# Performance work log

Measured on AMD Instinct MI355X. Metric: run time of the kernel, lower is better.

The kernel has to match this reference:

```python
import jax, jax.numpy as jnp
import numpy as np

B, D, H = 2048, 64, 512  # batch, state dim, vf hidden dim
IS_DIFFUSION = True      # vf output divided by 2.0 as in CNF.forward


def setup_inputs() -> dict:
    key = jax.random.key(0)
    ks = jax.random.split(key, 8)

    def lin(k, fi, fo):
        return jax.random.normal(k, (fi, fo), jnp.float32) / np.float32(np.sqrt(fi))

    return {
        "t": jax.random.uniform(ks[0], (1,), jnp.float32),      # scalar time, kept as [1]
        "x": jax.random.normal(ks[1], (B, D + 1), jnp.float32),  # last col = logp channel
        "W1": lin(ks[2], D + 1, H),
        "b1": jax.random.normal(ks[3], (H,), jnp.float32) * 0.01,
        "W2": lin(ks[4], H, H),
        "b2": jax.random.normal(ks[5], (H,), jnp.float32) * 0.01,
        "W3": lin(ks[6], H, D),
        "b3": jax.random.normal(ks[7], (D,), jnp.float32) * 0.01,
    }


def reference(t, x, W1, b1, W2, b2, W3, b3):
    scale = 2.0 if IS_DIFFUSION else 1.0
    xd = x[..., :-1]  # [B, D] -- drop augmented log-density channel

    def vf_single(xi):  # R^D -> R^D vector field, t and params closed over
        h = jnp.concatenate([xi, t])           # [D+1] (time-conditioned input)
        h = jnp.tanh(h @ W1 + b1)
        h = jnp.tanh(h @ W2 + b2)
        return (h @ W3 + b3) / scale

    dx = jax.vmap(vf_single)(xd)  # [B, D]
    # exact divergence: trace of per-sample Jacobian via reverse-mode (matches torch jacrev)
    div = jax.vmap(lambda xi: jnp.trace(jax.jacrev(vf_single)(xi)))(xd)  # [B]
    return jnp.concatenate([dx, div[:, None]], axis=-1)  # [B, D+1]
```

## Files before the change

### kernel.cpp

```cpp
#include <hip/hip_runtime.h>


constexpr int HD = 512;
constexpr int DD = 64;
constexpr int SB = 8;
constexpr int NB = 2048 / SB;

typedef __attribute__((ext_vector_type(8))) short bf16x8;
typedef __attribute__((ext_vector_type(4))) float f32x4;

__device__ inline unsigned short f2bf(float f) {
    union { float f; unsigned u; } v; v.f = f;
    return (unsigned short)((v.u + 0x7fffu + ((v.u >> 16) & 1u)) >> 16);
}
__device__ inline float fast_tanh(float xx) {
    float e = __expf(2.f * xx);
    return 1.f - 2.f / (e + 1.f);
}

__global__ __launch_bounds__(64) void cnf_pack_kernel(
    const float* __restrict__ W1, const float* __restrict__ W2,
    const float* __restrict__ W3, unsigned short* __restrict__ Bpack)
{
    __shared__ float w1s[64][33];
    __shared__ float w3s[16][65];
    const int b = blockIdx.x;
    const int mat = b >> 9, t = (b >> 4) & 31, kk = b & 15;
    const int l = threadIdx.x;
    const int q = l >> 4, nl = l & 15;
    const int n = t * 16 + nl;
    unsigned short o[8];
    if (mat == 0) {
#pragma unroll
        for (int j = 0; j < 8; ++j) {
            int k = kk * 32 + q * 8 + j;
            o[j] = f2bf(W2[k * HD + n]);
        }
    } else {
        for (int e = l; e < 64 * 32; e += 64) {
            int i = e >> 5, kl = e & 31;
            w1s[i][kl] = W1[i * HD + kk * 32 + kl];
        }
        for (int e = l; e < 16 * 64; e += 64) {
            int nn = e >> 6, i = e & 63;
            w3s[nn][i] = W3[(t * 16 + nn) * DD + i];
        }
        __syncthreads();
#pragma unroll
        for (int j = 0; j < 8; ++j) {
            int kl = q * 8 + j;
            float m = 0.f;
#pragma unroll 8
            for (int i = 0; i < 64; ++i) m += w1s[i][kl] * w3s[nl][i];
            o[j] = f2bf(W2[(kk * 32 + kl) * HD + n] * m);
        }
    }
    uint4 pk;
    pk.x = (unsigned)o[0] | ((unsigned)o[1] << 16);
    pk.y = (unsigned)o[2] | ((unsigned)o[3] << 16);
    pk.z = (unsigned)o[4] | ((unsigned)o[5] << 16);
    pk.w = (unsigned)o[6] | ((unsigned)o[7] << 16);
    reinterpret_cast<uint4*>(Bpack)[b * 64 + l] = pk;
}

__global__ __launch_bounds__(512, 2) void cnf_fused_kernel(
    const float* __restrict__ tptr, const float* __restrict__ x,
    const float* __restrict__ W1, const float* __restrict__ b1,
    const float* __restrict__ b2v, const float* __restrict__ W3,
    const float* __restrict__ b3, const unsigned short* __restrict__ Bpack,
    float* __restrict__ out)
{
    __shared__ float4 xsv[65 * 2];
    __shared__ unsigned short A_lds[16][520];
    __shared__ float4 h2v[HD * 2];
    __shared__ float4 divred[8][2];
    __shared__ float sm_b2[HD];

    const int tid  = threadIdx.x;
    const int s0   = blockIdx.x * SB;
    const int wave = tid >> 6, lane = tid & 63;

    {
        const float tval = tptr[0];
        for (int e = tid; e < SB * 65; e += 512) {
            int s = e / 65, i = e % 65;
            reinterpret_cast<float*>(xsv)[i * SB + s] =
                (i == DD) ? tval : x[(s0 + s) * 65 + i];
        }
        sm_b2[tid] = b2v[tid];
    }
    __syncthreads();

    {
        const int u = tid;
        const float bb = b1[u];
        float2 a0 = {bb, bb}, a1 = {bb, bb}, a2 = {bb, bb}, a3 = {bb, bb};
        for (int ib = 0; ib < 64; ib += 8) {
            float w[8];
#pragma unroll
            for (int qq = 0; qq < 8; ++qq) w[qq] = W1[(ib + qq) * HD + u];
#pragma unroll
            for (int qq = 0; qq < 8; ++qq) {
                float4 p = xsv[2 * (ib + qq)], r = xsv[2 * (ib + qq) + 1];
                a0.x += p.x * w[qq]; a0.y += p.y * w[qq];
                a1.x += p.z * w[qq]; a1.y += p.w * w[qq];
                a2.x += r.x * w[qq]; a2.y += r.y * w[qq];
                a3.x += r.z * w[qq]; a3.y += r.w * w[qq];
            }
        }
        {
            float w = W1[64 * HD + u];
            float4 p = xsv[128], r = xsv[129];
            a0.x += p.x * w; a0.y += p.y * w;
            a1.x += p.z * w; a1.y += p.w * w;
            a2.x += r.x * w; a2.y += r.y * w;
            a3.x += r.z * w; a3.y += r.w * w;
        }
        float h[8] = {fast_tanh(a0.x), fast_tanh(a0.y), fast_tanh(a1.x), fast_tanh(a1.y),
                      fast_tanh(a2.x), fast_tanh(a2.y), fast_tanh(a3.x), fast_tanh(a3.y)};
#pragma unroll
        for (int s = 0; s < 8; ++s) {
            A_lds[s][u]     = f2bf(h[s]);
            A_lds[8 + s][u] = f2bf(1.f - h[s] * h[s]);
        }
    }
    __syncthreads();

    f32x4 cw[4], cg[4];
#pragma unroll
    for (int i = 0; i < 4; ++i) { cw[i] = (f32x4){0,0,0,0}; cg[i] = (f32x4){0,0,0,0}; }
    {
        const unsigned short* arow = &A_lds[lane & 15][0];
        const int aoff = (lane >> 4) * 8;
        const bf16x8* bw = reinterpret_cast<const bf16x8*>(Bpack)
                         + (size_t)(wave * 64) * 64 + lane;
        const bf16x8* bg = bw + 32768;

        bf16x8 pA[16], pB[16];
        auto loadSB = [&](bf16x8* d, int kk) {
#pragma unroll
            for (int i = 0; i < 4; ++i) {
                d[i]      = bw[kk * 64 + i * 1024];
                d[4 + i]  = bg[kk * 64 + i * 1024];
                d[8 + i]  = bw[(kk + 1) * 64 + i * 1024];
                d[12 + i] = bg[(kk + 1) * 64 + i * 1024];
            }
        };
        auto mfmaSB = [&](const bf16x8* d, int kk) {
            bf16x8 af0 = *reinterpret_cast<const bf16x8*>(arow + kk * 32 + aoff);
#pragma unroll
            for (int i = 0; i < 4; ++i)
                cw[i] = __builtin_amdgcn_mfma_f32_16x16x32_bf16(af0, d[i], cw[i], 0, 0, 0);
#pragma unroll
            for (int i = 0; i < 4; ++i)
                cg[i] = __builtin_amdgcn_mfma_f32_16x16x32_bf16(af0, d[4 + i], cg[i], 0, 0, 0);
            bf16x8 af1 = *reinterpret_cast<const bf16x8*>(arow + (kk + 1) * 32 + aoff);
#pragma unroll
            for (int i = 0; i < 4; ++i)
                cw[i] = __builtin_amdgcn_mfma_f32_16x16x32_bf16(af1, d[8 + i], cw[i], 0, 0, 0);
#pragma unroll
            for (int i = 0; i < 4; ++i)
                cg[i] = __builtin_amdgcn_mfma_f32_16x16x32_bf16(af1, d[12 + i], cg[i], 0, 0, 0);
        };

        loadSB(pA, 0);
#pragma unroll
        for (int kb = 0; kb < 8; ++kb) {
            bf16x8* cur = (kb & 1) ? pB : pA;
            bf16x8* nxt = (kb & 1) ? pA : pB;
            if (kb < 7) loadSB(nxt, (kb + 1) * 2);
            mfmaSB(cur, kb * 2);
        }
    }

    {
        const int q = lane >> 4;
        const int src = (lane >= 32) ? lane - 32 : lane;
        float4 dp = {0.f, 0.f, 0.f, 0.f};
#pragma unroll
        for (int i = 0; i < 4; ++i) {
            const int m = wave * 64 + i * 16 + (lane & 15);
            const float bb = sm_b2[m];
            float4 hv;
            hv.x = fast_tanh(cw[i][0] + bb);
            hv.y = fast_tanh(cw[i][1] + bb);
            hv.z = fast_tanh(cw[i][2] + bb);
            hv.w = fast_tanh(cw[i][3] + bb);
            if (lane < 32) h2v[2 * m + q] = hv;
            float h0 = __shfl(hv.x, src), h1s = __shfl(hv.y, src);
            float h2s = __shfl(hv.z, src), h3s = __shfl(hv.w, src);
            dp.x += cg[i][0] * (1.f - h0 * h0);
            dp.y += cg[i][1] * (1.f - h1s * h1s);
            dp.z += cg[i][2] * (1.f - h2s * h2s);
            dp.w += cg[i][3] * (1.f - h3s * h3s);
        }
        if (lane >= 32) {
#pragma unroll
            for (int off = 8; off > 0; off >>= 1) {
                dp.x += __shfl_down(dp.x, off, 16);
                dp.y += __shfl_down(dp.y, off, 16);
                dp.z += __shfl_down(dp.z, off, 16);
                dp.w += __shfl_down(dp.w, off, 16);
            }
            if ((lane & 15) == 0) divred[wave][q - 2] = dp;
        }
    }
    __syncthreads();

    float* opart = reinterpret_cast<float*>(A_lds);

    {
        const int k = lane, part = wave;
        float o[8];
#pragma unroll
        for (int q = 0; q < 8; ++q) o[q] = 0.f;
        const int mb = part * 64;
        for (int mm = 0; mm < 64; mm += 4) {
            float w[4];
#pragma unroll
            for (int q = 0; q < 4; ++q) w[q] = W3[(mb + mm + q) * DD + k];
#pragma unroll
            for (int q = 0; q < 4; ++q) {
                const int m = mb + mm + q;
                float4 ha = h2v[2 * m], hb = h2v[2 * m + 1];
                o[0] += ha.x * w[q]; o[1] += ha.y * w[q];
                o[2] += ha.z * w[q]; o[3] += ha.w * w[q];
                o[4] += hb.x * w[q]; o[5] += hb.y * w[q];
                o[6] += hb.z * w[q]; o[7] += hb.w * w[q];
            }
        }
#pragma unroll
        for (int q = 0; q < 8; ++q) opart[part * 512 + q * 64 + k] = o[q];
    }
    __syncthreads();

    {
        const int s = tid >> 6, k = tid & 63;
        float sum = b3[k];
#pragma unroll
        for (int p = 0; p < 8; ++p) sum += opart[p * 512 + s * 64 + k];
        out[(s0 + s) * 65 + k] = 0.5f * sum;
    }
    if (tid < 8) {
        const int qq = tid >> 2, r = tid & 3;
        float ds = 0.f;
#pragma unroll
        for (int w = 0; w < 8; ++w)
            ds += reinterpret_cast<const float*>(&divred[w][qq])[r];
        out[(s0 + tid) * 65 + DD] = 0.5f * ds;
    }
}

extern "C" void kernel_launch(void* const* d_in, const int* in_sizes, int n_in,
                              void* d_out, int out_size, void* d_ws, size_t ws_size,
                              hipStream_t stream) {
    const float* t  = (const float*)d_in[0];
    const float* x  = (const float*)d_in[1];
    const float* W1 = (const float*)d_in[2];
    const float* b1 = (const float*)d_in[3];
    const float* W2 = (const float*)d_in[4];
    const float* b2 = (const float*)d_in[5];
    const float* W3 = (const float*)d_in[6];
    const float* b3 = (const float*)d_in[7];
    float* out = (float*)d_out;
    unsigned short* Bpack = (unsigned short*)d_ws;

    cnf_pack_kernel<<<1024, 64, 0, stream>>>(W1, W2, W3, Bpack);
    cnf_fused_kernel<<<NB, 512, 0, stream>>>(t, x, W1, b1, b2, W3, b3, Bpack, out);
}
```

Before: 97.81 us.

## Split hidden-layer output dimension across two blocks with atomic accumulation

Each sample group is now handled by two blocks, each computing half of the 512 second-layer hidden units plus their share of the divergence and output projection. Partial results are combined with atomicAdd into an output that is zeroed with a memset first. Launch bounds rise to four blocks per CU to pair with the smaller per-block register and LDS footprint. The aim is more blocks and better occupancy, at the cost of running the first layer twice per sample group, atomic traffic, and an extra memset launch.

```diff
diff --git a/kernel.cpp b/kernel.cpp
--- a/kernel.cpp
+++ b/kernel.cpp
@@ -4,7 +4,7 @@
 constexpr int HD = 512;
 constexpr int DD = 64;
 constexpr int SB = 8;
-constexpr int NB = 2048 / SB;
+constexpr int NBLK = 2 * 2048 / SB;
 
 typedef __attribute__((ext_vector_type(8))) short bf16x8;
 typedef __attribute__((ext_vector_type(4))) float f32x4;
@@ -63,7 +63,7 @@
     reinterpret_cast<uint4*>(Bpack)[b * 64 + l] = pk;
 }
 
-__global__ __launch_bounds__(512, 2) void cnf_fused_kernel(
+__global__ __launch_bounds__(512, 4) void cnf_fused_kernel(
     const float* __restrict__ tptr, const float* __restrict__ x,
     const float* __restrict__ W1, const float* __restrict__ b1,
     const float* __restrict__ b2v, const float* __restrict__ W3,
@@ -72,12 +72,14 @@
 {
     __shared__ float4 xsv[65 * 2];
     __shared__ unsigned short A_lds[16][520];
-    __shared__ float4 h2v[HD * 2];
+    __shared__ float4 h2v[256 * 2];
     __shared__ float4 divred[8][2];
-    __shared__ float sm_b2[HD];
+    __shared__ float sm_b2[256];
 
     const int tid  = threadIdx.x;
-    const int s0   = blockIdx.x * SB;
+    const int sg   = blockIdx.x >> 1;
+    const int q    = blockIdx.x & 1;
+    const int s0   = sg * SB;
     const int wave = tid >> 6, lane = tid & 63;
 
     {
@@ -87,7 +89,7 @@
             reinterpret_cast<float*>(xsv)[i * SB + s] =
                 (i == DD) ? tval : x[(s0 + s) * 65 + i];
         }
-        sm_b2[tid] = b2v[tid];
+        if (tid < 256) sm_b2[tid] = b2v[q * 256 + tid];
     }
     __syncthreads();
 
@@ -126,41 +128,39 @@
     }
     __syncthreads();
 
-    f32x4 cw[4], cg[4];
-#pragma unroll
-    for (int i = 0; i < 4; ++i) { cw[i] = (f32x4){0,0,0,0}; cg[i] = (f32x4){0,0,0,0}; }
+    f32x4 cw[2], cg[2];
+#pragma unroll
+    for (int i = 0; i < 2; ++i) { cw[i] = (f32x4){0,0,0,0}; cg[i] = (f32x4){0,0,0,0}; }
     {
         const unsigned short* arow = &A_lds[lane & 15][0];
         const int aoff = (lane >> 4) * 8;
+        const int t0 = q * 16 + wave * 2;
         const bf16x8* bw = reinterpret_cast<const bf16x8*>(Bpack)
-                         + (size_t)(wave * 64) * 64 + lane;
+                         + (size_t)(t0 * 16) * 64 + lane;
         const bf16x8* bg = bw + 32768;
 
-        bf16x8 pA[16], pB[16];
+        bf16x8 pA[8], pB[8];
         auto loadSB = [&](bf16x8* d, int kk) {
 #pragma unroll
-            for (int i = 0; i < 4; ++i) {
-                d[i]      = bw[kk * 64 + i * 1024];
-                d[4 + i]  = bg[kk * 64 + i * 1024];
-                d[8 + i]  = bw[(kk + 1) * 64 + i * 1024];
-                d[12 + i] = bg[(kk + 1) * 64 + i * 1024];
+            for (int v = 0; v < 2; ++v) {
+#pragma unroll
+                for (int i = 0; i < 2; ++i) {
+                    d[v * 4 + i]     = bw[(kk + v) * 64 + i * 1024];
+                    d[v * 4 + 2 + i] = bg[(kk + v) * 64 + i * 1024];
+                }
             }
         };
         auto mfmaSB = [&](const bf16x8* d, int kk) {
-            bf16x8 af0 = *reinterpret_cast<const bf16x8*>(arow + kk * 32 + aoff);
-#pragma unroll
-            for (int i = 0; i < 4; ++i)
-                cw[i] = __builtin_amdgcn_mfma_f32_16x16x32_bf16(af0, d[i], cw[i], 0, 0, 0);
-#pragma unroll
-            for (int i = 0; i < 4; ++i)
-                cg[i] = __builtin_amdgcn_mfma_f32_16x16x32_bf16(af0, d[4 + i], cg[i], 0, 0, 0);
-            bf16x8 af1 = *reinterpret_cast<const bf16x8*>(arow + (kk + 1) * 32 + aoff);
-#pragma unroll
-            for (int i = 0; i < 4; ++i)
-                cw[i] = __builtin_amdgcn_mfma_f32_16x16x32_bf16(af1, d[8 + i], cw[i], 0, 0, 0);
-#pragma unroll
-            for (int i = 0; i < 4; ++i)
-                cg[i] = __builtin_amdgcn_mfma_f32_16x16x32_bf16(af1, d[12 + i], cg[i], 0, 0, 0);
+#pragma unroll
+            for (int v = 0; v < 2; ++v) {
+                bf16x8 af = *reinterpret_cast<const bf16x8*>(arow + (kk + v) * 32 + aoff);
+#pragma unroll
+                for (int i = 0; i < 2; ++i)
+                    cw[i] = __builtin_amdgcn_mfma_f32_16x16x32_bf16(af, d[v * 4 + i], cw[i], 0, 0, 0);
+#pragma unroll
+                for (int i = 0; i < 2; ++i)
+                    cg[i] = __builtin_amdgcn_mfma_f32_16x16x32_bf16(af, d[v * 4 + 2 + i], cg[i], 0, 0, 0);
+            }
         };
 
         loadSB(pA, 0);
@@ -174,19 +174,19 @@
     }
 
     {
-        const int q = lane >> 4;
+        const int qd = lane >> 4;
         const int src = (lane >= 32) ? lane - 32 : lane;
         float4 dp = {0.f, 0.f, 0.f, 0.f};
 #pragma unroll
-        for (int i = 0; i < 4; ++i) {
-            const int m = wave * 64 + i * 16 + (lane & 15);
-            const float bb = sm_b2[m];
+        for (int i = 0; i < 2; ++i) {
+            const int ml = wave * 32 + i * 16 + (lane & 15);
+            const float bb = sm_b2[ml];
             float4 hv;
             hv.x = fast_tanh(cw[i][0] + bb);
             hv.y = fast_tanh(cw[i][1] + bb);
             hv.z = fast_tanh(cw[i][2] + bb);
             hv.w = fast_tanh(cw[i][3] + bb);
-            if (lane < 32) h2v[2 * m + q] = hv;
+            if (lane < 32) h2v[2 * ml + qd] = hv;
             float h0 = __shfl(hv.x, src), h1s = __shfl(hv.y, src);
             float h2s = __shfl(hv.z, src), h3s = __shfl(hv.w, src);
             dp.x += cg[i][0] * (1.f - h0 * h0);
@@ -202,7 +202,7 @@
                 dp.z += __shfl_down(dp.z, off, 16);
                 dp.w += __shfl_down(dp.w, off, 16);
             }
-            if ((lane & 15) == 0) divred[wave][q - 2] = dp;
+            if ((lane & 15) == 0) divred[wave][qd - 2] = dp;
         }
     }
     __syncthreads();
@@ -213,33 +213,34 @@
         const int k = lane, part = wave;
         float o[8];
 #pragma unroll
-        for (int q = 0; q < 8; ++q) o[q] = 0.f;
-        const int mb = part * 64;
-        for (int mm = 0; mm < 64; mm += 4) {
+        for (int qq = 0; qq < 8; ++qq) o[qq] = 0.f;
+        const int mb = part * 32;
+        for (int mm = 0; mm < 32; mm += 4) {
             float w[4];
 #pragma unroll
-            for (int q = 0; q < 4; ++q) w[q] = W3[(mb + mm + q) * DD + k];
-#pragma unroll
-            for (int q = 0; q < 4; ++q) {
-                const int m = mb + mm + q;
-                float4 ha = h2v[2 * m], hb = h2v[2 * m + 1];
-                o[0] += ha.x * w[q]; o[1] += ha.y * w[q];
-                o[2] += ha.z * w[q]; o[3] += ha.w * w[q];
-                o[4] += hb.x * w[q]; o[5] += hb.y * w[q];
-                o[6] += hb.z * w[q]; o[7] += hb.w * w[q];
-            }
-        }
-#pragma unroll
-        for (int q = 0; q < 8; ++q) opart[part * 512 + q * 64 + k] = o[q];
+            for (int j = 0; j < 4; ++j)
+                w[j] = W3[(q * 256 + mb + mm + j) * DD + k];
+#pragma unroll
+            for (int j = 0; j < 4; ++j) {
+                const int ml = mb + mm + j;
+                float4 ha = h2v[2 * ml], hb = h2v[2 * ml + 1];
+                o[0] += ha.x * w[j]; o[1] += ha.y * w[j];
+                o[2] += ha.z * w[j]; o[3] += ha.w * w[j];
+                o[4] += hb.x * w[j]; o[5] += hb.y * w[j];
+                o[6] += hb.z * w[j]; o[7] += hb.w * w[j];
+            }
+        }
+#pragma unroll
+        for (int qq = 0; qq < 8; ++qq) opart[part * 512 + qq * 64 + k] = o[qq];
     }
     __syncthreads();
 
     {
         const int s = tid >> 6, k = tid & 63;
-        float sum = b3[k];
+        float sum = (q == 0) ? b3[k] : 0.f;
 #pragma unroll
         for (int p = 0; p < 8; ++p) sum += opart[p * 512 + s * 64 + k];
-        out[(s0 + s) * 65 + k] = 0.5f * sum;
+        atomicAdd(&out[(s0 + s) * 65 + k], 0.5f * sum);
     }
     if (tid < 8) {
         const int qq = tid >> 2, r = tid & 3;
@@ -247,7 +248,7 @@
 #pragma unroll
         for (int w = 0; w < 8; ++w)
             ds += reinterpret_cast<const float*>(&divred[w][qq])[r];
-        out[(s0 + tid) * 65 + DD] = 0.5f * ds;
+        atomicAdd(&out[(s0 + tid) * 65 + DD], 0.5f * ds);
     }
 }
 
@@ -265,6 +266,7 @@
     float* out = (float*)d_out;
     unsigned short* Bpack = (unsigned short*)d_ws;
 
+    hipMemsetAsync(out, 0, (size_t)out_size * sizeof(float), stream);
     cnf_pack_kernel<<<1024, 64, 0, stream>>>(W1, W2, W3, Bpack);
-    cnf_fused_kernel<<<NB, 512, 0, stream>>>(t, x, W1, b1, b2, W3, b3, Bpack, out);
-}
+    cnf_fused_kernel<<<NBLK, 512, 0, stream>>>(t, x, W1, b1, b2, W3, b3, Bpack, out);
+}
```

Measured after the change: 98.57 us. No clear change (+0.8%).
